# Kernel optimization log

Hardware: AMD Instinct MI355X
Metric: run time of the kernel (lower is better)

Reference implementation:

```python
import jax, jax.numpy as jnp
import numpy as np

B, S, IX, OX, H = 4, 2048, 1024, 1024, 16
DH = OX // H  # head dim = 64


def setup_inputs() -> dict:
    key = jax.random.key(0)
    k1, k2, k3, k4, k5 = jax.random.split(key, 5)
    x = jax.random.normal(k1, (B, S, IX), dtype=jnp.float32)
    w1 = jax.random.normal(k2, (IX, 3 * OX), dtype=jnp.float32) * 0.02
    b1 = jnp.zeros((1, 3 * OX), dtype=jnp.float32)
    w2 = jax.random.normal(k3, (OX, IX), dtype=jnp.float32) * 0.02
    b2 = jnp.zeros((1, IX), dtype=jnp.float32)
    return {"x": x, "w1": w1, "b1": b1, "w2": w2, "b2": b2}


def _attention(x, w1, b1, w2, b2):
    # fused QKV projection: (B,S,IX) @ (IX,3*OX)
    qkv = jnp.einsum('bsi,io->bso', x, w1) + b1  # (B,S,3*OX)
    k, q, v = jnp.split(qkv, 3, axis=-1)  # NOTE original split order is k,q,v
    # split heads: (B,S,OX) -> (B,H,S,DH)
    def split_heads(t):
        return t.reshape(B, S, H, DH).transpose(0, 2, 1, 3)
    k, q, v = split_heads(k), split_heads(q), split_heads(v)
    # original code calls sdpa(k, q, v): scores = K @ Q^T / sqrt(DH)
    scores = jnp.einsum('bhsd,bhtd->bhst', k, q) / jnp.sqrt(jnp.float32(DH))
    attn = jax.nn.softmax(scores, axis=-1)  # (B,H,S,S)
    out = jnp.einsum('bhst,bhtd->bhsd', attn, v)  # (B,H,S,DH)
    # merge heads -> (B,S,OX)
    out = out.transpose(0, 2, 1, 3).reshape(B, S, OX)
    # output projection OX -> IX
    return jnp.einsum('bso,oi->bsi', out, w2) + b2


def reference(x, w1, b1, w2, b2):
    return _attention(x, w1, b1, w2, b2)
```

## Files before the change

kernel.cpp:

```cpp
#include <hip/hip_runtime.h>
#include <hip/hip_bf16.h>
#include <stdint.h>

#define B_   4
#define S_   2048
#define IX_  1024
#define OX_  1024
#define H_   16
#define DH_  64
#define MROWS (B_*S_)
#define NQKV  (3*OX_)

typedef __bf16 bf16x8 __attribute__((ext_vector_type(8)));
typedef float  f32x4  __attribute__((ext_vector_type(4)));

typedef __attribute__((address_space(1))) const uint8_t* gp_t;
typedef __attribute__((address_space(3))) uint8_t*       sp_t;

__device__ __forceinline__ void load_lds16(const void* g, void* s) {
  __builtin_amdgcn_global_load_lds((gp_t)g, (sp_t)s, 16, 0, 0);
}

__device__ __forceinline__ ushort f2bf(float f) {
  union { float f; uint32_t u; } x; x.f = f;
  uint32_t lsb = (x.u >> 16) & 1u;
  x.u += 0x7fffu + lsb;
  return (ushort)(x.u >> 16);
}

__device__ __forceinline__ uint32_t cvt_pk_bf16(float lo, float hi) {
  uint32_t r;
  asm("v_cvt_pk_bf16_f32 %0, %1, %2" : "=v"(r) : "v"(lo), "v"(hi));
  return r;
}

__global__ void cvt_bf16(const float* __restrict__ in, ushort* __restrict__ out, int n4) {
  int i = blockIdx.x * blockDim.x + threadIdx.x;
  if (i < n4) {
    float4 v = ((const float4*)in)[i];
    ushort4 o;
    o.x = f2bf(v.x); o.y = f2bf(v.y); o.z = f2bf(v.z); o.w = f2bf(v.w);
    ((ushort4*)out)[i] = o;
  }
}

__global__ void transpose_cvt(const float* __restrict__ in, ushort* __restrict__ out,
                              int K, int N) {
  __shared__ float tile[32][33];
  int n0 = blockIdx.x * 32, k0 = blockIdx.y * 32;
  int tx = threadIdx.x, ty = threadIdx.y;
  #pragma unroll
  for (int j = ty; j < 32; j += 8)
    tile[j][tx] = in[(size_t)(k0 + j) * N + n0 + tx];
  __syncthreads();
  #pragma unroll
  for (int j = ty; j < 32; j += 8)
    out[(size_t)(n0 + j) * K + k0 + tx] = f2bf(tile[tx][j]);
}

template<int OUTF32>
__global__ __launch_bounds__(256, 2) void gemm_bt(
    const ushort* __restrict__ A, const ushort* __restrict__ Bt,
    const float* __restrict__ bias, void* __restrict__ Cv,
    int M, int N, int K)
{
  __shared__ alignas(16) ushort As[128 * 32];
  __shared__ alignas(16) ushort Bs[128 * 32];
  const int t = threadIdx.x;
  const int wave = t >> 6, lane = t & 63;
  const int wr = wave >> 1, wc = wave & 1;
  const int lr = lane & 15, lk = (lane >> 4) * 8;
  const int brow = blockIdx.x * 128, bcol = blockIdx.y * 128;

  f32x4 acc[4][4] = {};

  for (int k0 = 0; k0 < K; k0 += 32) {
    #pragma unroll
    for (int i = 0; i < 2; ++i) {
      int chunk = wave * 128 + i * 64 + lane;
      int row = chunk >> 2, c8 = (chunk & 3) * 8;
      load_lds16(A  + (size_t)(brow + row) * K + k0 + c8, &As[(wave * 128 + i * 64) * 8]);
      load_lds16(Bt + (size_t)(bcol + row) * K + k0 + c8, &Bs[(wave * 128 + i * 64) * 8]);
    }
    __syncthreads();
    bf16x8 af[4], bfr[4];
    #pragma unroll
    for (int mi = 0; mi < 4; ++mi)
      af[mi] = *(const bf16x8*)&As[(wr * 64 + mi * 16 + lr) * 32 + lk];
    #pragma unroll
    for (int ni = 0; ni < 4; ++ni)
      bfr[ni] = *(const bf16x8*)&Bs[(wc * 64 + ni * 16 + lr) * 32 + lk];
    #pragma unroll
    for (int mi = 0; mi < 4; ++mi)
      #pragma unroll
      for (int ni = 0; ni < 4; ++ni)
        acc[mi][ni] = __builtin_amdgcn_mfma_f32_16x16x32_bf16(af[mi], bfr[ni], acc[mi][ni], 0, 0, 0);
    __syncthreads();
  }

  #pragma unroll
  for (int mi = 0; mi < 4; ++mi) {
    #pragma unroll
    for (int ni = 0; ni < 4; ++ni) {
      int col = bcol + wc * 64 + ni * 16 + lr;
      float bv = bias[col];
      #pragma unroll
      for (int j = 0; j < 4; ++j) {
        int row = brow + wr * 64 + mi * 16 + (lane >> 4) * 4 + j;
        float v = acc[mi][ni][j] + bv;
        if (OUTF32) ((float*)Cv)[(size_t)row * N + col] = v;
        else        ((ushort*)Cv)[(size_t)row * N + col] = f2bf(v);
      }
    }
  }
}

__global__ __launch_bounds__(256, 3) void flash_attn(
    const ushort* __restrict__ qkv, ushort* __restrict__ out)
{
  __shared__ alignas(16) ushort Ks[2][64 * 64];
  __shared__ alignas(16) ushort Vs[2][64 * 64];
  __shared__ alignas(16) ushort Ps[128 * 64];

  const int t = threadIdx.x;
  const int wave = t >> 6, lane = t & 63;
  const int lr = lane & 15, lg = lane >> 4;
  const int bx = blockIdx.x;
  const int bh = blockIdx.y;
  const int b = bh >> 4, h = bh & 15;

  const size_t base = (size_t)b * S_ * NQKV;
  const ushort* Kg = qkv + base + h * DH_;
  const ushort* Qg = qkv + base + OX_ + h * DH_;
  const ushort* Vg = qkv + base + 2 * OX_ + h * DH_;
  const int s0 = bx * 128;

  const int vt0 = (t >> 3) * 2;
  const int vd8 = (t & 7) * 8;

  #pragma unroll
  for (int i = 0; i < 2; ++i) {
    int chunk = i * 256 + t;
    int row = chunk >> 3;
    int cg = (chunk & 7) ^ (row & 7);
    load_lds16(Qg + (size_t)row * NQKV + cg * 8, &Ks[0][chunk * 8]);
  }
  uint4 v0 = *(const uint4*)(Vg + (size_t)vt0 * NQKV + vd8);
  uint4 v1 = *(const uint4*)(Vg + (size_t)(vt0 + 1) * NQKV + vd8);
  #pragma unroll
  for (int i = 0; i < 4; ++i) {
    int chunk = wave * 256 + i * 64 + lane;
    int row = chunk >> 3;
    int cg = (chunk & 7) ^ (row & 7);
    load_lds16(Kg + (size_t)(s0 + row) * NQKV + cg * 8, &Ps[chunk * 8]);
  }
  __syncthreads();

  bf16x8 aq[2][2];
  #pragma unroll
  for (int si = 0; si < 2; ++si)
    #pragma unroll
    for (int kk = 0; kk < 2; ++kk) {
      int r = wave * 32 + si * 16 + lr;
      aq[si][kk] = *(const bf16x8*)&Ps[r * 64 + (((kk * 4 + lg) ^ (r & 7)) * 8)];
    }

  {
    #pragma unroll
    for (int j = 0; j < 8; ++j) {
      uint32_t a = ((const uint32_t*)&v0)[j >> 1];
      uint32_t bb = ((const uint32_t*)&v1)[j >> 1];
      uint32_t lo = (j & 1) ? (a >> 16) : (a & 0xffffu);
      uint32_t hi = (j & 1) ? (bb >> 16) : (bb & 0xffffu);
      int d = vd8 + j;
      int ch = (vt0 >> 3) ^ ((d ^ (d >> 3)) & 7);
      *(uint32_t*)((uint8_t*)&Vs[0][0] + d * 128 + ch * 16 + ((vt0 >> 1) & 3) * 4)
          = lo | (hi << 16);
    }
  }
  __syncthreads();

  f32x4 oT[4][2] = {};
  float lrun[2] = {};

  for (int kt = 0; kt < 32; ++kt) {
    const int cur = kt & 1;
    const int t0n = (kt + 1) * 64;
    uint4 v0n, v1n;
    if (kt < 31) {
      #pragma unroll
      for (int i = 0; i < 2; ++i) {
        int chunk = i * 256 + t;
        int row = chunk >> 3;
        int cg = (chunk & 7) ^ (row & 7);
        load_lds16(Qg + (size_t)(t0n + row) * NQKV + cg * 8, &Ks[cur ^ 1][chunk * 8]);
      }
      v0n = *(const uint4*)(Vg + (size_t)(t0n + vt0) * NQKV + vd8);
      v1n = *(const uint4*)(Vg + (size_t)(t0n + vt0 + 1) * NQKV + vd8);
    }

    f32x4 sT[4][2] = {};
    __builtin_amdgcn_s_setprio(1);
    #pragma unroll
    for (int kk = 0; kk < 2; ++kk) {
      #pragma unroll
      for (int ti = 0; ti < 4; ++ti) {
        int rt = ti * 16 + lr;
        bf16x8 ak = *(const bf16x8*)&Ks[cur][rt * 64 + (((kk * 4 + lg) ^ (rt & 7)) * 8)];
        #pragma unroll
        for (int si = 0; si < 2; ++si)
          sT[ti][si] = __builtin_amdgcn_mfma_f32_16x16x32_bf16(ak, aq[si][kk], sT[ti][si], 0, 0, 0);
      }
    }
    __builtin_amdgcn_s_setprio(0);

    #pragma unroll
    for (int si = 0; si < 2; ++si) {
      int s_loc = wave * 32 + si * 16 + lr;
      int sx = s_loc & 7;
      #pragma unroll
      for (int ti = 0; ti < 4; ++ti) {
        float p0 = __expf(sT[ti][si][0] * 0.125f);
        float p1 = __expf(sT[ti][si][1] * 0.125f);
        float p2 = __expf(sT[ti][si][2] * 0.125f);
        float p3 = __expf(sT[ti][si][3] * 0.125f);
        lrun[si] += (p0 + p1) + (p2 + p3);
        uint32_t u0 = cvt_pk_bf16(p0, p1);
        uint32_t u1 = cvt_pk_bf16(p2, p3);
        int p = ti * 8 + lg * 2;
        uint8_t* dst = (uint8_t*)Ps + s_loc * 128 + (((p >> 2) ^ sx) * 16) + (p & 3) * 4;
        *(uint2*)dst = make_uint2(u0, u1);
      }
    }

    __builtin_amdgcn_s_setprio(1);
    #pragma unroll
    for (int kk = 0; kk < 2; ++kk) {
      bf16x8 bp[2];
      #pragma unroll
      for (int si = 0; si < 2; ++si) {
        int s_loc = wave * 32 + si * 16 + lr;
        bp[si] = *(const bf16x8*)&Ps[s_loc * 64 + (((kk * 4 + lg) ^ (s_loc & 7)) * 8)];
      }
      #pragma unroll
      for (int nd = 0; nd < 4; ++nd) {
        int dr = nd * 16 + lr;
        int ch = (kk * 4 + lg) ^ ((dr ^ (dr >> 3)) & 7);
        bf16x8 av = *(const bf16x8*)&Vs[cur][dr * 64 + ch * 8];
        #pragma unroll
        for (int si = 0; si < 2; ++si)
          oT[nd][si] = __builtin_amdgcn_mfma_f32_16x16x32_bf16(av, bp[si], oT[nd][si], 0, 0, 0);
      }
    }
    __builtin_amdgcn_s_setprio(0);

    if (kt < 31) {
      #pragma unroll
      for (int j = 0; j < 8; ++j) {
        uint32_t a = ((const uint32_t*)&v0n)[j >> 1];
        uint32_t bb = ((const uint32_t*)&v1n)[j >> 1];
        uint32_t lo = (j & 1) ? (a >> 16) : (a & 0xffffu);
        uint32_t hi = (j & 1) ? (bb >> 16) : (bb & 0xffffu);
        int d = vd8 + j;
        int ch = (vt0 >> 3) ^ ((d ^ (d >> 3)) & 7);
        *(uint32_t*)((uint8_t*)&Vs[cur ^ 1][0] + d * 128 + ch * 16 + ((vt0 >> 1) & 3) * 4)
            = lo | (hi << 16);
      }
    }
    __syncthreads();
  }

  float linv[2];
  #pragma unroll
  for (int si = 0; si < 2; ++si) {
    float s = lrun[si];
    s += __shfl_xor(s, 16, 64);
    s += __shfl_xor(s, 32, 64);
    linv[si] = 1.0f / s;
  }

  #pragma unroll
  for (int nd = 0; nd < 4; ++nd) {
    #pragma unroll
    for (int si = 0; si < 2; ++si) {
      float w0 = oT[nd][si][0] * linv[si];
      float w1 = oT[nd][si][1] * linv[si];
      float w2 = oT[nd][si][2] * linv[si];
      float w3 = oT[nd][si][3] * linv[si];
      uint32_t u0 = cvt_pk_bf16(w0, w1);
      uint32_t u1 = cvt_pk_bf16(w2, w3);
      int row = s0 + wave * 32 + si * 16 + lr;
      int col = h * DH_ + nd * 16 + lg * 4;
      *(uint2*)&out[(size_t)(b * S_ + row) * OX_ + col] = make_uint2(u0, u1);
    }
  }
}

extern "C" void kernel_launch(void* const* d_in, const int* in_sizes, int n_in,
                              void* d_out, int out_size, void* d_ws, size_t ws_size,
                              hipStream_t stream) {
  const float* x  = (const float*)d_in[0];
  const float* w1 = (const float*)d_in[1];
  const float* b1 = (const float*)d_in[2];
  const float* w2 = (const float*)d_in[3];
  const float* b2 = (const float*)d_in[4];
  float* out = (float*)d_out;
  uint8_t* ws = (uint8_t*)d_ws;

  ushort* xb   = (ushort*)(ws);
  ushort* w1t  = (ushort*)(ws + 16777216);
  ushort* w2t  = (ushort*)(ws + 23068672);
  ushort* qkv  = (ushort*)(ws + 25165824);
  ushort* attn = (ushort*)(ws + 75497472);

  hipLaunchKernelGGL(cvt_bf16, dim3(8192), dim3(256), 0, stream, x, xb, MROWS * IX_ / 4);
  hipLaunchKernelGGL(transpose_cvt, dim3(NQKV / 32, IX_ / 32), dim3(32, 8), 0, stream,
                     w1, w1t, IX_, NQKV);
  hipLaunchKernelGGL(transpose_cvt, dim3(IX_ / 32, OX_ / 32), dim3(32, 8), 0, stream,
                     w2, w2t, OX_, IX_);
  hipLaunchKernelGGL((gemm_bt<0>), dim3(MROWS / 128, NQKV / 128), dim3(256), 0, stream,
                     xb, w1t, b1, (void*)qkv, MROWS, NQKV, IX_);
  hipLaunchKernelGGL(flash_attn, dim3(S_ / 128, B_ * H_), dim3(256), 0, stream, qkv, attn);
  hipLaunchKernelGGL((gemm_bt<1>), dim3(MROWS / 128, IX_ / 128), dim3(256), 0, stream,
                     attn, w2t, b2, (void*)out, MROWS, IX_, OX_);
}
```

Baseline: 301.4 us.

## Use 256x256-tile 8-wave pipelined GEMM for QKV projection

Replaces the 128x128 QKV projection GEMM with a new 512-thread kernel that computes 256x256 output tiles. It uses double-buffered LDS staged in quarter-tiles via direct global-to-LDS loads, interleaves those loads across eight MFMA phases with raised wave priority, and remaps block IDs for L2 locality. The goal is more reuse of each loaded tile and better overlap of memory traffic with compute. In exchange it uses large LDS (128KB) and many accumulator registers, with hand-written vmcnt waits that must match the load ordering.

```diff
diff --git a/kernel.cpp b/kernel.cpp
--- a/kernel.cpp
+++ b/kernel.cpp
@@ -115,6 +115,129 @@
   }
 }
 
+__global__ __launch_bounds__(512, 2) void gemm8p(
+    const ushort* __restrict__ A, const ushort* __restrict__ Bt,
+    const float* __restrict__ bias, ushort* __restrict__ C,
+    int M, int N, int K)
+{
+  __shared__ alignas(16) ushort As[2][256 * 64];
+  __shared__ alignas(16) ushort Bs[2][256 * 64];
+  const int t = threadIdx.x;
+  const int wid = t >> 6, lane = t & 63;
+  const int wr = wid >> 2, wc = wid & 3;
+  const int lr = lane & 15, lg = lane >> 4;
+
+  const int cpx = gridDim.x >> 3;
+  const int bid = blockIdx.x;
+  const int swz = (bid & 7) * cpx + (bid >> 3);
+  const int nbx = M >> 8;
+  const int bx = swz % nbx, by = swz / nbx;
+  const int brow = bx * 256, bcol = by * 256;
+
+  const ushort* Ag = A  + (size_t)brow * K;
+  const ushort* Bg = Bt + (size_t)bcol * K;
+
+  f32x4 acc[8][4] = {};
+  const int NT = K >> 7;
+
+  auto stageA = [&](int buf, int kt, int q) {
+    #pragma unroll
+    for (int i = 0; i < 2; ++i) {
+      int u = i * 512 + t;
+      int urow = u >> 3, c = u & 7;
+      int row = ((urow >> 6) << 7) + (q << 6) + (urow & 63);
+      int cg = c ^ (row & 7);
+      load_lds16(Ag + (size_t)row * K + kt * 64 + cg * 8, &As[buf][row * 64 + c * 8]);
+    }
+  };
+  auto stageB = [&](int buf, int kt, int q) {
+    #pragma unroll
+    for (int i = 0; i < 2; ++i) {
+      int u = i * 512 + t;
+      int urow = u >> 3, c = u & 7;
+      int row = ((urow >> 5) << 6) + (q << 5) + (urow & 31);
+      int cg = c ^ (row & 7);
+      load_lds16(Bg + (size_t)row * K + kt * 64 + cg * 8, &Bs[buf][row * 64 + c * 8]);
+    }
+  };
+
+  stageA(0, 0, 0); stageB(0, 0, 0); stageA(0, 0, 1); stageB(0, 0, 1);
+  stageA(1, 1, 0); stageB(1, 1, 0);
+  asm volatile("s_waitcnt vmcnt(4)" ::: "memory");
+  __builtin_amdgcn_s_barrier();
+
+  for (int it = 0; it < NT; ++it) {
+    const bool last = (it == NT - 1);
+    #pragma unroll
+    for (int p = 0; p < 8; ++p) {
+      const int buf = p >> 2;
+      const int miQ = (p & 3) >> 1, niP = p & 1;
+
+      bf16x8 af[4][2], bfr[2][2];
+      #pragma unroll
+      for (int m4 = 0; m4 < 4; ++m4) {
+        int r = wr * 128 + (miQ * 4 + m4) * 16 + lr;
+        #pragma unroll
+        for (int kk = 0; kk < 2; ++kk)
+          af[m4][kk] = *(const bf16x8*)&As[buf][r * 64 + ((kk * 4 + lg) ^ (r & 7)) * 8];
+      }
+      #pragma unroll
+      for (int n2 = 0; n2 < 2; ++n2) {
+        int r = wc * 64 + (niP * 2 + n2) * 16 + lr;
+        #pragma unroll
+        for (int kk = 0; kk < 2; ++kk)
+          bfr[n2][kk] = *(const bf16x8*)&Bs[buf][r * 64 + ((kk * 4 + lg) ^ (r & 7)) * 8];
+      }
+
+      if (p == 0)              stageA(1, 2 * it + 1, 1);
+      else if (p == 1)         stageB(1, 2 * it + 1, 1);
+      else if (!last) {
+        if      (p == 2)       stageA(0, 2 * it + 2, 0);
+        else if (p == 3)       stageB(0, 2 * it + 2, 0);
+        else if (p == 4)       stageA(0, 2 * it + 2, 1);
+        else if (p == 5)       stageB(0, 2 * it + 2, 1);
+        else if (p == 6)       stageA(1, 2 * it + 3, 0);
+        else if (p == 7)       stageB(1, 2 * it + 3, 0);
+      }
+
+      __builtin_amdgcn_s_barrier();
+      __builtin_amdgcn_s_setprio(1);
+      #pragma unroll
+      for (int m4 = 0; m4 < 4; ++m4)
+        #pragma unroll
+        for (int n2 = 0; n2 < 2; ++n2)
+          #pragma unroll
+          for (int kk = 0; kk < 2; ++kk)
+            acc[miQ * 4 + m4][niP * 2 + n2] =
+              __builtin_amdgcn_mfma_f32_16x16x32_bf16(af[m4][kk], bfr[n2][kk],
+                                                      acc[miQ * 4 + m4][niP * 2 + n2], 0, 0, 0);
+      __builtin_amdgcn_s_setprio(0);
+
+      if (p == 3) {
+        if (last) asm volatile("s_waitcnt vmcnt(0)" ::: "memory");
+        else      asm volatile("s_waitcnt vmcnt(4)" ::: "memory");
+      } else if (p == 7 && !last) {
+        asm volatile("s_waitcnt vmcnt(4)" ::: "memory");
+      }
+      __builtin_amdgcn_s_barrier();
+    }
+  }
+
+  #pragma unroll
+  for (int ni = 0; ni < 4; ++ni) {
+    int col = bcol + wc * 64 + ni * 16 + lr;
+    float bv = bias[col];
+    #pragma unroll
+    for (int mi = 0; mi < 8; ++mi) {
+      #pragma unroll
+      for (int j = 0; j < 4; ++j) {
+        int row = brow + wr * 128 + mi * 16 + lg * 4 + j;
+        C[(size_t)row * N + col] = f2bf(acc[mi][ni][j] + bv);
+      }
+    }
+  }
+}
+
 __global__ __launch_bounds__(256, 3) void flash_attn(
     const ushort* __restrict__ qkv, ushort* __restrict__ out)
 {
@@ -318,8 +441,8 @@
                      w1, w1t, IX_, NQKV);
   hipLaunchKernelGGL(transpose_cvt, dim3(IX_ / 32, OX_ / 32), dim3(32, 8), 0, stream,
                      w2, w2t, OX_, IX_);
-  hipLaunchKernelGGL((gemm_bt<0>), dim3(MROWS / 128, NQKV / 128), dim3(256), 0, stream,
-                     xb, w1t, b1, (void*)qkv, MROWS, NQKV, IX_);
+  hipLaunchKernelGGL(gemm8p, dim3((MROWS / 256) * (NQKV / 256)), dim3(512), 0, stream,
+                     xb, w1t, b1, qkv, MROWS, NQKV, IX_);
   hipLaunchKernelGGL(flash_attn, dim3(S_ / 128, B_ * H_), dim3(256), 0, stream, qkv, attn);
   hipLaunchKernelGGL((gemm_bt<1>), dim3(MROWS / 128, IX_ / 128), dim3(256), 0, stream,
                      attn, w2t, b2, (void*)out, MROWS, IX_, OX_);
```

Result: slower. 322.1 us (+6.9%).
